# Performance work log

Measured on AMD Instinct MI355X. Metric: run time of the kernel, lower is better.

Reference implementation:

```python
import jax, jax.numpy as jnp
import numpy as np

D_MODEL = 64  # scale denominator, per init_kwargs
B, S, H, D = 4, 2048, 16, 64


def setup_inputs() -> dict:
    key = jax.random.key(0)
    kq, kk, kv, km = jax.random.split(key, 4)
    q = jax.random.normal(kq, (B, S, H, D), dtype=jnp.float32)
    k = jax.random.normal(kk, (B, S, H, D), dtype=jnp.float32)
    v = jax.random.normal(kv, (B, S, H, D), dtype=jnp.float32)
    mask = jax.random.randint(km, (B, H, S, S), 0, 2, dtype=jnp.int32)
    return {"q": q, "k": k, "v": v, "mask": mask}


def reference(q, k, v, mask):
    # scores: [b, h, q, k]
    scores = jnp.einsum('bqhd,bkhd->bhqk', q, k)
    scores = scores / jnp.sqrt(jnp.asarray(D_MODEL, dtype=scores.dtype))
    # Faithful to original: masked positions set to 1e-20 (not -inf) pre-softmax
    scores = jnp.where(mask == 0, jnp.asarray(1e-20, dtype=scores.dtype), scores)
    attn = jax.nn.softmax(scores, axis=-1)
    # output: [b, q, h, d]
    return jnp.einsum('bhqk,bkhd->bqhd', attn, v)
```

## Files before the change

kernel.cpp:

```cpp
#include <hip/hip_runtime.h>


typedef __attribute__((ext_vector_type(8))) short short8;
typedef __attribute__((ext_vector_type(4))) float f32x4;
typedef __attribute__((ext_vector_type(4))) int   i32x4;
typedef unsigned int       u32;
typedef unsigned long long u64;

#define MFMA(a, b, c) __builtin_amdgcn_mfma_f32_16x16x32_bf16((a), (b), (c), 0, 0, 0)

static __device__ __forceinline__ short f2bf(float f) {
    __bf16 h = (__bf16)f;
    return __builtin_bit_cast(short, h);
}

constexpr int S_ = 2048, HD_ = 1024, STEPS_ = 32;
constexpr long KP_ELEMS = 64L * 32 * 4 * 2 * 64 * 8;

__global__ __launch_bounds__(256) void prepack_kv(const float* __restrict__ K,
                                                  const float* __restrict__ V,
                                                  short* __restrict__ Kp,
                                                  short* __restrict__ Vp) {
    int t = blockIdx.x * 256 + threadIdx.x;
    int lane = t & 63, hf = (t >> 6) & 1, kt = (t >> 7) & 3, step = (t >> 9) & 31, bh = t >> 14;
    int g = lane >> 4, c = lane & 15, b = bh >> 4, h = bh & 15;

    {
        int row = step * 64 + kt * 16 + c;
        const float* src = K + (long)(b * S_ + row) * HD_ + h * 64 + hf * 32 + g * 8;
        f32x4 x0 = *(const f32x4*)src, x1 = *(const f32x4*)(src + 4);
        short8 o;
        o[0] = f2bf(x0[0]); o[1] = f2bf(x0[1]); o[2] = f2bf(x0[2]); o[3] = f2bf(x0[3]);
        o[4] = f2bf(x1[0]); o[5] = f2bf(x1[1]); o[6] = f2bf(x1[2]); o[7] = f2bf(x1[3]);
        *(short8*)(Kp + (long)t * 8) = o;
    }
    {
        int col = kt * 16 + c, row0 = step * 64 + hf * 32;
        const float* vb = V + (long)(b * S_) * HD_ + h * 64 + col;
        short8 o;
#pragma unroll
        for (int i = 0; i < 8; ++i) {
            int row = row0 + ((i < 4) ? g * 4 + i : 16 + g * 4 + (i - 4));
            o[i] = f2bf(vb[(long)row * HD_]);
        }
        *(short8*)(Vp + (long)t * 8) = o;
    }
}

__global__ __launch_bounds__(256, 2)
void attn_fused2(const float* __restrict__ Q, const short* __restrict__ Kp,
                 const short* __restrict__ Vp, const int* __restrict__ M,
                 float* __restrict__ O)
{
    const float QSCALE = 0.125f * 1.44269504088896340736f;

    __shared__ u32 sbits[16384];

    int orig = blockIdx.x;
    int wg   = (orig & 7) * 64 + (orig >> 3);
    int bh   = wg >> 3, qb = wg & 7;
    int b    = bh >> 4, h = bh & 15;

    int lane = threadIdx.x & 63, wave = threadIdx.x >> 6;
    int g = lane >> 4, c = lane & 15;
    int q0 = qb * 256 + wave * 64;

    u32* sw = sbits + wave * 4096;

    const float* qbase = Q + (long)(b * S_) * HD_ + h * 64;
    const int*   mbase = M + ((long)bh << 22);
    float*       obase = O + (long)(b * S_) * HD_ + h * 64;
    const short* kpb   = Kp + (long)bh * STEPS_ * 4096;
    const short* vpb   = Vp + (long)bh * STEPS_ * 4096;

    short8 qf[4][2];
#pragma unroll
    for (int qt = 0; qt < 4; ++qt) {
        const float* qr = qbase + (long)(q0 + qt * 16 + c) * HD_;
#pragma unroll
        for (int hf = 0; hf < 2; ++hf) {
            f32x4 x0 = *(const f32x4*)(qr + hf * 32 + g * 8);
            f32x4 x1 = *(const f32x4*)(qr + hf * 32 + g * 8 + 4);
            short8 t;
            t[0] = f2bf(x0[0] * QSCALE); t[1] = f2bf(x0[1] * QSCALE);
            t[2] = f2bf(x0[2] * QSCALE); t[3] = f2bf(x0[3] * QSCALE);
            t[4] = f2bf(x1[0] * QSCALE); t[5] = f2bf(x1[1] * QSCALE);
            t[6] = f2bf(x1[2] * QSCALE); t[7] = f2bf(x1[3] * QSCALE);
            qf[qt][hf] = t;
        }
    }

    {
        const int* mr = mbase + ((long)q0 << 11) + lane * 4;
#pragma unroll 2
        for (int row = 0; row < 64; ++row) {
            const int* rp = mr + ((long)row << 11);
            u32 w = 0;
#pragma unroll
            for (int j = 0; j < 8; ++j) {
                i32x4 m = __builtin_nontemporal_load((const i32x4*)(rp + j * 256));
                w |= (m[0] != 0 ? 1u : 0u) << (j * 4);
                w |= (m[1] != 0 ? 1u : 0u) << (j * 4 + 1);
                w |= (m[2] != 0 ? 1u : 0u) << (j * 4 + 2);
                w |= (m[3] != 0 ? 1u : 0u) << (j * 4 + 3);
            }
            sw[row * 64 + ((lane + row * 4) & 63)] = w;
        }
    }

    f32x4 acc[4][4];
#pragma unroll
    for (int qt = 0; qt < 4; ++qt)
#pragma unroll
        for (int dt = 0; dt < 4; ++dt) acc[qt][dt] = (f32x4){0.f, 0.f, 0.f, 0.f};
    float lsum[4] = {0.f, 0.f, 0.f, 0.f};

#pragma unroll 1
    for (int step = 0; step < STEPS_; ++step) {
        const short* kp = kpb + (long)step * 4096;
        const short* vp = vpb + (long)step * 4096;
        short8 kf[4][2], vf[4][2];
#pragma unroll
        for (int kt = 0; kt < 4; ++kt)
#pragma unroll
            for (int hf = 0; hf < 2; ++hf) {
                kf[kt][hf] = *(const short8*)(kp + ((kt * 2 + hf) * 64 + lane) * 8);
                vf[kt][hf] = *(const short8*)(vp + ((kt * 2 + hf) * 64 + lane) * 8);
            }

        int wbase = (step & 3) * 16 + g;
        int shft  = (step >> 2) * 4;

#pragma unroll
        for (int qt = 0; qt < 4; ++qt) {
            f32x4 st[4];
#pragma unroll
            for (int kt = 0; kt < 4; ++kt) {
                f32x4 z = (f32x4){0.f, 0.f, 0.f, 0.f};
                z = MFMA(kf[kt][0], qf[qt][0], z);
                z = MFMA(kf[kt][1], qf[qt][1], z);
                st[kt] = z;
            }

            int row = qt * 16 + c;
            u32 fld[4];
#pragma unroll
            for (int kt = 0; kt < 4; ++kt) {
                int w = wbase + kt * 4;
                fld[kt] = sw[row * 64 + ((w + row * 4) & 63)] >> shft;
            }

            float p[4][4];
            float s = 0.f;
#pragma unroll
            for (int kt = 0; kt < 4; ++kt) {
#pragma unroll
                for (int r = 0; r < 4; ++r) {
                    u32 bit = (fld[kt] >> r) & 1u;
                    float val = bit ? st[kt][r] : 0.0f;
                    float e = exp2f(val);
                    p[kt][r] = e;
                    s += e;
                }
            }
            lsum[qt] += s;

            short8 pb0, pb1;
            pb0[0] = f2bf(p[0][0]); pb0[1] = f2bf(p[0][1]); pb0[2] = f2bf(p[0][2]); pb0[3] = f2bf(p[0][3]);
            pb0[4] = f2bf(p[1][0]); pb0[5] = f2bf(p[1][1]); pb0[6] = f2bf(p[1][2]); pb0[7] = f2bf(p[1][3]);
            pb1[0] = f2bf(p[2][0]); pb1[1] = f2bf(p[2][1]); pb1[2] = f2bf(p[2][2]); pb1[3] = f2bf(p[2][3]);
            pb1[4] = f2bf(p[3][0]); pb1[5] = f2bf(p[3][1]); pb1[6] = f2bf(p[3][2]); pb1[7] = f2bf(p[3][3]);

#pragma unroll
            for (int dt = 0; dt < 4; ++dt) {
                acc[qt][dt] = MFMA(vf[dt][0], pb0, acc[qt][dt]);
                acc[qt][dt] = MFMA(vf[dt][1], pb1, acc[qt][dt]);
            }
        }
    }

#pragma unroll
    for (int qt = 0; qt < 4; ++qt) {
        float t0 = lsum[qt];
        t0 += __shfl_xor(t0, 16);
        t0 += __shfl_xor(t0, 32);
        float inv = 1.0f / t0;
        float* orow = obase + (long)(q0 + qt * 16 + c) * HD_;
#pragma unroll
        for (int dt = 0; dt < 4; ++dt) {
            f32x4 o = acc[qt][dt] * inv;
            __builtin_nontemporal_store(o, (f32x4*)(orow + dt * 16 + g * 4));
        }
    }
}

__global__ __launch_bounds__(256, 2)
void attn_fwd(const float* __restrict__ Q, const float* __restrict__ K,
              const float* __restrict__ V, const int* __restrict__ M,
              float* __restrict__ O)
{
    const float QSCALE = 0.125f * 1.44269504088896340736f;
    int orig = blockIdx.x;
    int wg   = (orig & 7) * 64 + (orig >> 3);
    int bh   = wg >> 3, qb = wg & 7;
    int b    = bh >> 4, h = bh & 15;
    int lane = threadIdx.x & 63, wave = threadIdx.x >> 6;
    int g = lane >> 4, c = lane & 15;
    int q0 = qb * 256 + wave * 64;

    const float* qbase = Q + (long)(b * S_) * HD_ + h * 64;
    const float* kbase = K + (long)(b * S_) * HD_ + h * 64;
    const float* vbase = V + (long)(b * S_) * HD_ + h * 64;
    const int*   mbase = M + ((long)bh << 22);
    float*       obase = O + (long)(b * S_) * HD_ + h * 64;

    short8 qf[4][2];
#pragma unroll
    for (int qt = 0; qt < 4; ++qt) {
        const float* qr = qbase + (long)(q0 + qt * 16 + c) * HD_;
#pragma unroll
        for (int hf = 0; hf < 2; ++hf) {
            f32x4 x0 = *(const f32x4*)(qr + hf * 32 + g * 8);
            f32x4 x1 = *(const f32x4*)(qr + hf * 32 + g * 8 + 4);
            short8 t;
            t[0] = f2bf(x0[0] * QSCALE); t[1] = f2bf(x0[1] * QSCALE);
            t[2] = f2bf(x0[2] * QSCALE); t[3] = f2bf(x0[3] * QSCALE);
            t[4] = f2bf(x1[0] * QSCALE); t[5] = f2bf(x1[1] * QSCALE);
            t[6] = f2bf(x1[2] * QSCALE); t[7] = f2bf(x1[3] * QSCALE);
            qf[qt][hf] = t;
        }
    }

    f32x4 acc[4][4];
#pragma unroll
    for (int qt = 0; qt < 4; ++qt)
#pragma unroll
        for (int dt = 0; dt < 4; ++dt) acc[qt][dt] = (f32x4){0.f, 0.f, 0.f, 0.f};
    float lsum[4] = {0.f, 0.f, 0.f, 0.f};

#pragma unroll 1
    for (int step = 0; step < STEPS_; ++step) {
        int kv0 = step * 64;
        short8 kf[4][2];
#pragma unroll
        for (int kt = 0; kt < 4; ++kt) {
            const float* kr = kbase + (long)(kv0 + kt * 16 + c) * HD_;
#pragma unroll
            for (int hf = 0; hf < 2; ++hf) {
                f32x4 x0 = *(const f32x4*)(kr + hf * 32 + g * 8);
                f32x4 x1 = *(const f32x4*)(kr + hf * 32 + g * 8 + 4);
                short8 t;
                t[0] = f2bf(x0[0]); t[1] = f2bf(x0[1]); t[2] = f2bf(x0[2]); t[3] = f2bf(x0[3]);
                t[4] = f2bf(x1[0]); t[5] = f2bf(x1[1]); t[6] = f2bf(x1[2]); t[7] = f2bf(x1[3]);
                kf[kt][hf] = t;
            }
        }
        short8 vf[4][2];
#pragma unroll
        for (int hf = 0; hf < 2; ++hf) {
            const float* vr[8];
#pragma unroll
            for (int i = 0; i < 4; ++i) {
                vr[i]     = vbase + (long)(kv0 + hf * 32 + g * 4 + i) * HD_ + c;
                vr[4 + i] = vbase + (long)(kv0 + hf * 32 + 16 + g * 4 + i) * HD_ + c;
            }
#pragma unroll
            for (int dt = 0; dt < 4; ++dt) {
                short8 t;
#pragma unroll
                for (int i = 0; i < 8; ++i) t[i] = f2bf(vr[i][dt * 16]);
                vf[dt][hf] = t;
            }
        }
#pragma unroll
        for (int qt = 0; qt < 4; ++qt) {
            f32x4 st[4];
#pragma unroll
            for (int kt = 0; kt < 4; ++kt) {
                f32x4 z = (f32x4){0.f, 0.f, 0.f, 0.f};
                z = MFMA(kf[kt][0], qf[qt][0], z);
                z = MFMA(kf[kt][1], qf[qt][1], z);
                st[kt] = z;
            }
            const int* mrp = mbase + ((long)(q0 + qt * 16 + c) << 11) + kv0 + g * 4;
            float p[4][4];
            float s = 0.f;
#pragma unroll
            for (int kt = 0; kt < 4; ++kt) {
                i32x4 mkv = *(const i32x4*)(mrp + kt * 16);
#pragma unroll
                for (int r = 0; r < 4; ++r) {
                    float val = (mkv[r] != 0) ? st[kt][r] : 0.0f;
                    float e = exp2f(val);
                    p[kt][r] = e;
                    s += e;
                }
            }
            lsum[qt] += s;
            short8 pb0, pb1;
            pb0[0] = f2bf(p[0][0]); pb0[1] = f2bf(p[0][1]); pb0[2] = f2bf(p[0][2]); pb0[3] = f2bf(p[0][3]);
            pb0[4] = f2bf(p[1][0]); pb0[5] = f2bf(p[1][1]); pb0[6] = f2bf(p[1][2]); pb0[7] = f2bf(p[1][3]);
            pb1[0] = f2bf(p[2][0]); pb1[1] = f2bf(p[2][1]); pb1[2] = f2bf(p[2][2]); pb1[3] = f2bf(p[2][3]);
            pb1[4] = f2bf(p[3][0]); pb1[5] = f2bf(p[3][1]); pb1[6] = f2bf(p[3][2]); pb1[7] = f2bf(p[3][3]);
#pragma unroll
            for (int dt = 0; dt < 4; ++dt) {
                acc[qt][dt] = MFMA(vf[dt][0], pb0, acc[qt][dt]);
                acc[qt][dt] = MFMA(vf[dt][1], pb1, acc[qt][dt]);
            }
        }
    }
#pragma unroll
    for (int qt = 0; qt < 4; ++qt) {
        float t0 = lsum[qt];
        t0 += __shfl_xor(t0, 16);
        t0 += __shfl_xor(t0, 32);
        float inv = 1.0f / t0;
        float* orow = obase + (long)(q0 + qt * 16 + c) * HD_;
#pragma unroll
        for (int dt = 0; dt < 4; ++dt) {
            f32x4 o = acc[qt][dt] * inv;
            *(f32x4*)(orow + dt * 16 + g * 4) = o;
        }
    }
}

extern "C" void kernel_launch(void* const* d_in, const int* in_sizes, int n_in,
                              void* d_out, int out_size, void* d_ws, size_t ws_size,
                              hipStream_t stream) {
    const float* q = (const float*)d_in[0];
    const float* k = (const float*)d_in[1];
    const float* v = (const float*)d_in[2];
    const int*   m = (const int*)d_in[3];
    float* out = (float*)d_out;

    size_t need = (size_t)2 * KP_ELEMS * sizeof(short);
    if (ws_size >= need) {
        short* Kp = (short*)d_ws;
        short* Vp = Kp + KP_ELEMS;
        prepack_kv<<<dim3(4096), dim3(256), 0, stream>>>(k, v, Kp, Vp);
        attn_fused2<<<dim3(512), dim3(256), 0, stream>>>(q, Kp, Vp, m, out);
    } else {
        attn_fwd<<<dim3(512), dim3(256), 0, stream>>>(q, k, v, m, out);
    }
}
```

Baseline: 299.8 us.

## Stream mask bits in double-buffered chunks overlapped with attention compute

Instead of loading the whole 64x2048 mask tile per wave into LDS before the main loop, the kernel now loads only the first 256-column chunk up front. It prefetches the next chunk's mask into registers during each step and packs it into a double-buffered LDS region after the MFMAs. This halves LDS use and hides most of the mask-read latency (the dominant memory traffic) behind compute. The cost is sixteen extra i32x4 registers per thread for the prefetch, which could raise register pressure and lower occupancy.

Result: slower. 514.5 us (+71.6%).

```diff
diff --git a/kernel.cpp b/kernel.cpp
--- a/kernel.cpp
+++ b/kernel.cpp
@@ -12,6 +12,11 @@
 static __device__ __forceinline__ short f2bf(float f) {
     __bf16 h = (__bf16)f;
     return __builtin_bit_cast(short, h);
+}
+
+static __device__ __forceinline__ u32 nib4(i32x4 m) {
+    return (m[0] != 0 ? 1u : 0u) | (m[1] != 0 ? 2u : 0u) |
+           (m[2] != 0 ? 4u : 0u) | (m[3] != 0 ? 8u : 0u);
 }
 
 constexpr int S_ = 2048, HD_ = 1024, STEPS_ = 32;
@@ -48,13 +53,13 @@
 }
 
 __global__ __launch_bounds__(256, 2)
-void attn_fused2(const float* __restrict__ Q, const short* __restrict__ Kp,
+void attn_fused3(const float* __restrict__ Q, const short* __restrict__ Kp,
                  const short* __restrict__ Vp, const int* __restrict__ M,
                  float* __restrict__ O)
 {
     const float QSCALE = 0.125f * 1.44269504088896340736f;
 
-    __shared__ u32 sbits[16384];
+    __shared__ u32 sbits[8192];
 
     int orig = blockIdx.x;
     int wg   = (orig & 7) * 64 + (orig >> 3);
@@ -65,7 +70,7 @@
     int g = lane >> 4, c = lane & 15;
     int q0 = qb * 256 + wave * 64;
 
-    u32* sw = sbits + wave * 4096;
+    u32* sw = sbits + wave * 2048;
 
     const float* qbase = Q + (long)(b * S_) * HD_ + h * 64;
     const int*   mbase = M + ((long)bh << 22);
@@ -92,19 +97,16 @@
 
     {
         const int* mr = mbase + ((long)q0 << 11) + lane * 4;
-#pragma unroll 2
-        for (int row = 0; row < 64; ++row) {
-            const int* rp = mr + ((long)row << 11);
+#pragma unroll 4
+        for (int rg = 0; rg < 16; ++rg) {
             u32 w = 0;
 #pragma unroll
-            for (int j = 0; j < 8; ++j) {
-                i32x4 m = __builtin_nontemporal_load((const i32x4*)(rp + j * 256));
-                w |= (m[0] != 0 ? 1u : 0u) << (j * 4);
-                w |= (m[1] != 0 ? 1u : 0u) << (j * 4 + 1);
-                w |= (m[2] != 0 ? 1u : 0u) << (j * 4 + 2);
-                w |= (m[3] != 0 ? 1u : 0u) << (j * 4 + 3);
-            }
-            sw[row * 64 + ((lane + row * 4) & 63)] = w;
+            for (int rr = 0; rr < 4; ++rr) {
+                i32x4 m = __builtin_nontemporal_load(
+                    (const i32x4*)(mr + ((long)(rg * 4 + rr) << 11)));
+                w |= nib4(m) << (rr * 8);
+            }
+            sw[rg * 64 + ((lane + rg * 4) & 63)] = w;
         }
     }
 
@@ -115,8 +117,14 @@
         for (int dt = 0; dt < 4; ++dt) acc[qt][dt] = (f32x4){0.f, 0.f, 0.f, 0.f};
     float lsum[4] = {0.f, 0.f, 0.f, 0.f};
 
+    int shft = (c & 3) * 8;
+
 #pragma unroll 1
     for (int step = 0; step < STEPS_; ++step) {
+        int j    = step >> 2;
+        int sL   = step & 3;
+        int bufr = (j & 1) << 10;
+
         const short* kp = kpb + (long)step * 4096;
         const short* vp = vpb + (long)step * 4096;
         short8 kf[4][2], vf[4][2];
@@ -128,8 +136,16 @@
                 vf[kt][hf] = *(const short8*)(vp + ((kt * 2 + hf) * 64 + lane) * 8);
             }
 
-        int wbase = (step & 3) * 16 + g;
-        int shft  = (step >> 2) * 4;
+        i32x4 pm[16];
+        bool pre = (j < 7);
+        if (pre) {
+            const int* mc = mbase + ((long)q0 << 11) + (j + 1) * 256 + lane * 4;
+#pragma unroll
+            for (int t = 0; t < 16; ++t)
+                pm[t] = __builtin_nontemporal_load(
+                    (const i32x4*)(mc + ((long)(sL * 16 + t) << 11)));
+        }
+        __builtin_amdgcn_sched_barrier(0);
 
 #pragma unroll
         for (int qt = 0; qt < 4; ++qt) {
@@ -142,12 +158,12 @@
                 st[kt] = z;
             }
 
-            int row = qt * 16 + c;
+            int rgq = qt * 4 + (c >> 2);
             u32 fld[4];
 #pragma unroll
             for (int kt = 0; kt < 4; ++kt) {
-                int w = wbase + kt * 4;
-                fld[kt] = sw[row * 64 + ((w + row * 4) & 63)] >> shft;
+                int lw = sL * 16 + kt * 4 + g;
+                fld[kt] = sw[bufr + rgq * 64 + ((lw + rgq * 4) & 63)] >> shft;
             }
 
             float p[4][4];
@@ -175,6 +191,19 @@
             for (int dt = 0; dt < 4; ++dt) {
                 acc[qt][dt] = MFMA(vf[dt][0], pb0, acc[qt][dt]);
                 acc[qt][dt] = MFMA(vf[dt][1], pb1, acc[qt][dt]);
+            }
+        }
+
+        if (pre) {
+            int bufw = ((j + 1) & 1) << 10;
+#pragma unroll
+            for (int t4 = 0; t4 < 4; ++t4) {
+                int rg = sL * 4 + t4;
+                u32 w = 0;
+#pragma unroll
+                for (int rr = 0; rr < 4; ++rr)
+                    w |= nib4(pm[t4 * 4 + rr]) << (rr * 8);
+                sw[bufw + rg * 64 + ((lane + rg * 4) & 63)] = w;
             }
         }
     }
@@ -338,7 +367,7 @@
         short* Kp = (short*)d_ws;
         short* Vp = Kp + KP_ELEMS;
         prepack_kv<<<dim3(4096), dim3(256), 0, stream>>>(k, v, Kp, Vp);
-        attn_fused2<<<dim3(512), dim3(256), 0, stream>>>(q, Kp, Vp, m, out);
+        attn_fused3<<<dim3(512), dim3(256), 0, stream>>>(q, Kp, Vp, m, out);
     } else {
         attn_fwd<<<dim3(512), dim3(256), 0, stream>>>(q, k, v, m, out);
     }
```
